# Performance work log

Measured on AMD Instinct MI355X. Metric: run time of the kernel, lower is better.

The kernel has to match this reference:

```python
import jax, jax.numpy as jnp
import numpy as np

K = 16  # neighbors
EPS = 1e-3  # Keras BatchNormalization default epsilon


def _bn(x, gamma, beta, mean, var):
    return (x - mean) * jax.lax.rsqrt(var + EPS) * gamma + beta


def setup_inputs() -> dict:
    key = jax.random.key(0)
    ks = jax.random.split(key, 16)
    B, P, C = 128, 256, 64
    inp = {
        "points": jax.random.normal(ks[0], (B, P, 3), jnp.float32),
        "features": jax.random.normal(ks[1], (B, P, C), jnp.float32),
        "w0": jax.random.normal(ks[2], (2 * C, 64), jnp.float32) * 0.08,
        "w1": jax.random.normal(ks[3], (64, 64), jnp.float32) * 0.12,
        "w2": jax.random.normal(ks[4], (64, 64), jnp.float32) * 0.12,
        "gammas": 0.8 + 0.4 * jax.random.uniform(ks[5], (3, 64), jnp.float32),
        "betas": 0.1 * jax.random.normal(ks[6], (3, 64), jnp.float32),
        "means": 0.1 * jax.random.normal(ks[7], (3, 64), jnp.float32),
        "variances": 0.5 + jax.random.uniform(ks[8], (3, 64), jnp.float32),
        "sc_w": jax.random.normal(ks[9], (C, 64), jnp.float32) * 0.12,
        "sc_gamma": 0.8 + 0.4 * jax.random.uniform(ks[10], (64,), jnp.float32),
        "sc_beta": 0.1 * jax.random.normal(ks[11], (64,), jnp.float32),
        "sc_mean": 0.1 * jax.random.normal(ks[12], (64,), jnp.float32),
        "sc_var": 0.5 + jax.random.uniform(ks[13], (64,), jnp.float32),
    }
    return inp


def reference(points, features, w0, w1, w2, gammas, betas, means, variances,
              sc_w, sc_gamma, sc_beta, sc_mean, sc_var):
    B, P, C = features.shape
    # pairwise squared-distance matrix: ||a||^2 - 2 a.b + ||b||^2  -> [B, P, P]
    r = jnp.sum(points * points, axis=2, keepdims=True)  # [B, P, 1]
    m = jnp.einsum('bpc,bqc->bpq', points, points)
    d = r - 2.0 * m + jnp.swapaxes(r, 1, 2)
    # top_k of -d: K+1 nearest (incl. self at position 0), drop self
    _, idx = jax.lax.top_k(-d, K + 1)
    idx = idx[:, :, 1:]  # [B, P, K]
    # KNN gather of features
    knn_fts = features[jnp.arange(B)[:, None, None], idx]  # [B, P, K, C]
    center = jnp.broadcast_to(features[:, :, None, :], (B, P, K, C))
    x = jnp.concatenate([center, knn_fts - center], axis=-1)  # [B, P, K, 2C]
    # per-edge MLP: 1x1 conv + BN (inference) + relu
    for i, w in enumerate((w0, w1, w2)):
        x = jnp.einsum('bpkc,cd->bpkd', x, w)
        x = _bn(x, gammas[i], betas[i], means[i], variances[i])
        x = jax.nn.relu(x)
    fts = jnp.mean(x, axis=2)  # average pooling over neighbors -> [B, P, 64]
    # shortcut 1x1 conv + BN
    sc = jnp.einsum('bpc,cd->bpd', features, sc_w)
    sc = _bn(sc, sc_gamma, sc_beta, sc_mean, sc_var)
    return jax.nn.relu(sc + fts)
```

## Files before the change

kernel.cpp:

```cpp
#include <hip/hip_runtime.h>
#include <math.h>

#define NBATCH 128
#define NP 256
#define NC 64
#define KNN 16
#define EPSV 1e-3f

typedef __bf16 bf16_t;
typedef bf16_t bf16x8 __attribute__((ext_vector_type(8)));
typedef float f32x4 __attribute__((ext_vector_type(4)));
typedef unsigned short u16x4 __attribute__((ext_vector_type(4)));

static __device__ __forceinline__ f32x4 mfma16(bf16x8 a, bf16x8 b, f32x4 c) {
    return __builtin_amdgcn_mfma_f32_16x16x32_bf16(a, b, c, 0, 0, 0);
}
static __device__ __forceinline__ unsigned short f2bfu(float f) {
    union { bf16_t b; unsigned short u; } cv; cv.b = (bf16_t)f; return cv.u;
}
static __device__ __forceinline__ unsigned umin2(unsigned a, unsigned b) { return a < b ? a : b; }
static __device__ __forceinline__ unsigned umax2(unsigned a, unsigned b) { return a > b ? a : b; }

#define CFENCE() asm volatile("" ::: "memory")

#define INSERTK(k_)                                                   \
    do {                                                              \
        _Pragma("unroll")                                             \
        for (int ii = KNN - 1; ii >= 1; --ii)                         \
            bk[ii] = umin2(umax2((k_), bk[ii - 1]), bk[ii]);          \
        bk[0] = umin2((k_), bk[0]);                                   \
    } while (0)

__global__ __launch_bounds__(256) void setup_kernel(
    const float* __restrict__ points, const float* __restrict__ features,
    const float* __restrict__ w0, const float* __restrict__ w1,
    const float* __restrict__ w2, const float* __restrict__ sc_w,
    const float* __restrict__ gammas, const float* __restrict__ betas,
    const float* __restrict__ means, const float* __restrict__ variances,
    const float* __restrict__ sc_gamma, const float* __restrict__ sc_beta,
    const float* __restrict__ sc_mean, const float* __restrict__ sc_var,
    unsigned short* __restrict__ fbf, unsigned short* __restrict__ wsf,
    float* __restrict__ bnp, int* __restrict__ knn_out)
{
    const int bid = blockIdx.x;
    if (bid < 1024) {
        const int tid = bid * 256 + threadIdx.x;
        const float4 a = ((const float4*)features)[tid * 2];
        const float4 b = ((const float4*)features)[tid * 2 + 1];
        union { unsigned short s[8]; uint4 v; } r;
        r.s[0] = f2bfu(a.x); r.s[1] = f2bfu(a.y); r.s[2] = f2bfu(a.z); r.s[3] = f2bfu(a.w);
        r.s[4] = f2bfu(b.x); r.s[5] = f2bfu(b.y); r.s[6] = f2bfu(b.z); r.s[7] = f2bfu(b.w);
        ((uint4*)fbf)[tid] = r.v;
    } else if (bid < 1105) {
        const int tid = (bid - 1024) * 256 + threadIdx.x;
        if (tid < 20480) {
            const int region = tid >> 12;
            const int e2 = tid & 4095;
            const int f = e2 >> 9;
            const int r = e2 & 511;
            const int lane = r >> 3, j = r & 7;
            const int ks = f >> 2, t = f & 3;
            const int row = ks * 32 + (lane >> 4) * 8 + j;
            const int col = 4 * (lane & 15) + t;
            float v;
            if (region == 0)      v = w0[row * 64 + col] - w0[(64 + row) * 64 + col];
            else if (region == 1) v = w0[(64 + row) * 64 + col];
            else if (region == 2) v = w1[row * 64 + col];
            else if (region == 3) v = w2[row * 64 + col];
            else                  v = sc_w[row * 64 + col];
            wsf[tid] = f2bfu(v);
        } else {
            const int e = tid - 20480;
            if (e < 192) {
                float s = gammas[e] * rsqrtf(variances[e] + EPSV);
                bnp[e] = s;
                bnp[192 + e] = betas[e] - means[e] * s;
            } else if (e < 256) {
                const int d = e - 192;
                float s = sc_gamma[d] * rsqrtf(sc_var[d] + EPSV);
                bnp[384 + d] = s;
                bnp[448 + d] = sc_beta[d] - sc_mean[d] * s;
            }
        }
    } else {
        __shared__ __align__(16) float4 sp[NP];
        __shared__ unsigned sk[128][17];
        const int kb = bid - 1105;
        const int bb = kb >> 1;
        const int qbase = (kb & 1) * 128;
        const int t = threadIdx.x;
        const int qt = t & 127;
        const int half = t >> 7;
        const int p = qbase + qt;

        const float* pb = points + (size_t)bb * NP * 3;
        sp[t] = make_float4(pb[t * 3 + 0], pb[t * 3 + 1], pb[t * 3 + 2], 0.f);
        __syncthreads();

        const float4 qp = sp[p];
        unsigned bk[KNN];
#pragma unroll
        for (int i = 0; i < KNN; ++i) bk[i] = 0xFFFFFFFFu;

        const int cbase = half * 128;
#pragma unroll 4
        for (int c = 0; c < 128; ++c) {
            const int cand = cbase + c;
            const float4 P = sp[cand];
            const float dx = qp.x - P.x, dy = qp.y - P.y, dz = qp.z - P.z;
            const float d = fmaf(dx, dx, fmaf(dy, dy, dz * dz));
            unsigned key = (__float_as_uint(d) & 0xFFFFFF00u) | (unsigned)cand;
            key = (cand == p) ? 0xFFFFFFFFu : key;
            INSERTK(key);
        }

        if (half == 1) {
#pragma unroll
            for (int i = 0; i < KNN; ++i) sk[qt][i] = bk[i];
        }
        __syncthreads();
        if (half == 0) {
            for (int j = 0; j < KNN; ++j) {
                const unsigned key = sk[qt][j];
                if (key >= bk[KNN - 1]) break;
                INSERTK(key);
            }
            int* op = knn_out + ((size_t)bb * NP + p) * KNN;
#pragma unroll
            for (int i = 0; i < KNN; ++i) op[i] = (int)(bk[i] & 0xFFu);
        }
    }
}

__global__ __launch_bounds__(256) void edge_kernel(
    const unsigned short* __restrict__ fbf, const int* __restrict__ knn_idx,
    const unsigned short* __restrict__ wsf, const float* __restrict__ bnp,
    float* __restrict__ out)
{
    __shared__ __align__(16) unsigned short wlds[24 * 512];
    __shared__ __align__(16) unsigned short slab[4][16 * 72];
    __shared__ __align__(16) float s0buf[4][8][64];
    __shared__ __align__(16) float ftsbuf[4][8][64];

    const int tid = threadIdx.x;
    const int wid = tid >> 6;
    const int l = tid & 63;
    const int i = l & 15;
    const int h = l >> 4;
    const int wg = (blockIdx.x & 7) * 128 + (blockIdx.x >> 3);
    const int p0 = (wg * 4 + wid) * 8;
    const int b = p0 >> 8;

    unsigned short* sl = slab[wid];

    {
        const uint4* src = (const uint4*)(wsf + 4096);
        uint4* dst = (uint4*)wlds;
#pragma unroll
        for (int k = 0; k < 6; ++k) dst[tid + k * 256] = src[tid + k * 256];
    }

    #define WF(fi_) (*(const bf16x8*)&wlds[(fi_) * 512 + l * 8])

    float4 scl[3], shf[3];
#pragma unroll
    for (int L = 0; L < 3; ++L) {
        scl[L] = *(const float4*)&bnp[L * 64 + 4 * i];
        shf[L] = *(const float4*)&bnp[192 + L * 64 + 4 * i];
    }

    {
        const bf16x8* __restrict__ WV = (const bf16x8*)(wsf);
        const unsigned short* cp = fbf + (size_t)(p0 + (i & 7)) * NC;
        bf16x8 a0 = *(const bf16x8*)(cp + 8 * h);
        bf16x8 a1 = *(const bf16x8*)(cp + 32 + 8 * h);
        f32x4 acc[4];
#pragma unroll
        for (int t = 0; t < 4; ++t) {
            f32x4 z = {0.f, 0.f, 0.f, 0.f};
            z = mfma16(a0, WV[t * 64 + l], z);
            acc[t] = mfma16(a1, WV[(4 + t) * 64 + l], z);
        }
        if (h < 2) {
#pragma unroll
            for (int r = 0; r < 4; ++r) {
                float4 v = make_float4(acc[0][r], acc[1][r], acc[2][r], acc[3][r]);
                *(float4*)&s0buf[wid][h * 4 + r][4 * i] = v;
            }
        }
    }
    int nks[8];
#pragma unroll
    for (int q = 0; q < 8; ++q) nks[q] = knn_idx[(size_t)(p0 + q) * KNN + i];

    __syncthreads();

    bf16x8 fc0, fc1;
    {
        const unsigned short* sp = fbf + (size_t)(b * NP + nks[0]) * NC;
        fc0 = *(const bf16x8*)(sp + 8 * h);
        fc1 = *(const bf16x8*)(sp + 32 + 8 * h);
    }

#pragma unroll
    for (int q = 0; q < 8; ++q) {
        float4 s0q = *(const float4*)&s0buf[wid][q][4 * i];
        {
            f32x4 acc[4];
#pragma unroll
            for (int t = 0; t < 4; ++t) {
                f32x4 z = {0.f, 0.f, 0.f, 0.f};
                z = mfma16(fc0, WF(t), z);
                acc[t] = mfma16(fc1, WF(4 + t), z);
            }
            const float* sp_ = (const float*)&s0q;
            const float* sc_ = (const float*)&scl[0];
            const float* sh_ = (const float*)&shf[0];
#pragma unroll
            for (int r = 0; r < 4; ++r) {
                u16x4 pk;
#pragma unroll
                for (int t = 0; t < 4; ++t)
                    pk[t] = f2bfu(fmaxf(fmaf(acc[t][r] + sp_[t], sc_[t], sh_[t]), 0.f));
                *(u16x4*)&sl[(h * 4 + r) * 72 + 4 * i] = pk;
            }
        }
        bf16x8 fn0, fn1;
        if (q < 7) {
            const unsigned short* sp = fbf + (size_t)(b * NP + nks[(q + 1) & 7]) * NC;
            fn0 = *(const bf16x8*)(sp + 8 * h);
            fn1 = *(const bf16x8*)(sp + 32 + 8 * h);
        }
        CFENCE();

        {
            bf16x8 x0 = *(const bf16x8*)(sl + i * 72 + h * 8);
            bf16x8 x1 = *(const bf16x8*)(sl + i * 72 + h * 8 + 32);
            f32x4 acc[4];
#pragma unroll
            for (int t = 0; t < 4; ++t) {
                f32x4 z = {0.f, 0.f, 0.f, 0.f};
                z = mfma16(x0, WF(8 + t), z);
                acc[t] = mfma16(x1, WF(12 + t), z);
            }
            const float* sc_ = (const float*)&scl[1];
            const float* sh_ = (const float*)&shf[1];
#pragma unroll
            for (int r = 0; r < 4; ++r) {
                u16x4 pk;
#pragma unroll
                for (int t = 0; t < 4; ++t)
                    pk[t] = f2bfu(fmaxf(fmaf(acc[t][r], sc_[t], sh_[t]), 0.f));
                *(u16x4*)&sl[(h * 4 + r) * 72 + 4 * i] = pk;
            }
        }
        CFENCE();

        {
            bf16x8 x0 = *(const bf16x8*)(sl + i * 72 + h * 8);
            bf16x8 x1 = *(const bf16x8*)(sl + i * 72 + h * 8 + 32);
            const float* sc_ = (const float*)&scl[2];
            const float* sh_ = (const float*)&shf[2];
            float st[4];
#pragma unroll
            for (int t = 0; t < 4; ++t) {
                f32x4 z = {0.f, 0.f, 0.f, 0.f};
                z = mfma16(x0, WF(16 + t), z);
                f32x4 acc = mfma16(x1, WF(20 + t), z);
                float s = 0.f;
#pragma unroll
                for (int r = 0; r < 4; ++r)
                    s += fmaxf(fmaf(acc[r], sc_[t], sh_[t]), 0.f);
                s += __shfl_xor(s, 16, 64);
                s += __shfl_xor(s, 32, 64);
                st[t] = s * (1.f / 16.f);
            }
            if (h == 0)
                *(float4*)&ftsbuf[wid][q][4 * i] =
                    make_float4(st[0], st[1], st[2], st[3]);
        }
        CFENCE();
        fc0 = fn0; fc1 = fn1;
    }

    {
        const bf16x8* __restrict__ WS = (const bf16x8*)(wsf + 16384);
        float4 sscl = *(const float4*)&bnp[384 + 4 * i];
        float4 sshf = *(const float4*)&bnp[448 + 4 * i];
        const unsigned short* fp = fbf + (size_t)(p0 + (i & 7)) * NC;
        bf16x8 a0 = *(const bf16x8*)(fp + 8 * h);
        bf16x8 a1 = *(const bf16x8*)(fp + 32 + 8 * h);
        f32x4 acc[4];
#pragma unroll
        for (int t = 0; t < 4; ++t) {
            f32x4 z = {0.f, 0.f, 0.f, 0.f};
            z = mfma16(a0, WS[t * 64 + l], z);
            acc[t] = mfma16(a1, WS[(4 + t) * 64 + l], z);
        }
        if (h < 2) {
            const float* ss_ = (const float*)&sscl;
            const float* sf_ = (const float*)&sshf;
#pragma unroll
            for (int r = 0; r < 4; ++r) {
                const int q = h * 4 + r;
                float4 fts = *(const float4*)&ftsbuf[wid][q][4 * i];
                const float* ft_ = (const float*)&fts;
                float4 o;
                float* o_ = (float*)&o;
#pragma unroll
                for (int t = 0; t < 4; ++t)
                    o_[t] = fmaxf(fmaf(acc[t][r], ss_[t], sf_[t]) + ft_[t], 0.f);
                *(float4*)&out[(size_t)(p0 + q) * NC + 4 * i] = o;
            }
        }
    }
    #undef WF
}

extern "C" void kernel_launch(void* const* d_in, const int* in_sizes, int n_in,
                              void* d_out, int out_size, void* d_ws, size_t ws_size,
                              hipStream_t stream) {
    const float* points    = (const float*)d_in[0];
    const float* features  = (const float*)d_in[1];
    const float* w0        = (const float*)d_in[2];
    const float* w1        = (const float*)d_in[3];
    const float* w2        = (const float*)d_in[4];
    const float* gammas    = (const float*)d_in[5];
    const float* betas     = (const float*)d_in[6];
    const float* means     = (const float*)d_in[7];
    const float* variances = (const float*)d_in[8];
    const float* sc_w      = (const float*)d_in[9];
    const float* sc_gamma  = (const float*)d_in[10];
    const float* sc_beta   = (const float*)d_in[11];
    const float* sc_mean   = (const float*)d_in[12];
    const float* sc_var    = (const float*)d_in[13];
    float* out = (float*)d_out;

    int* knn_buf = (int*)d_ws;
    unsigned short* fbf = (unsigned short*)((char*)d_ws + (1 << 21));
    unsigned short* wsf = (unsigned short*)((char*)d_ws + (3 << 21));
    float* bnp = (float*)((char*)d_ws + (3 << 21) + 40960);

    setup_kernel<<<1361, 256, 0, stream>>>(points, features, w0, w1, w2, sc_w,
                                           gammas, betas, means, variances,
                                           sc_gamma, sc_beta, sc_mean, sc_var,
                                           fbf, wsf, bnp, knn_buf);
    edge_kernel<<<NBATCH * NP / 32, 256, 0, stream>>>(fbf, knn_buf, wsf, bnp, out);
}
```

Baseline: 46.99 us.

## Fold BN scales into weights and chain MFMA layers in registers without LDS slab

The BN scales for layers 2 and 3 are folded into the next layer's weights, and the layer biases are pre-divided by the scale so they can seed the MFMA accumulators. The operand roles are swapped (weights as A, activations as B) and the output channels are permuted so each layer's MFMA output can be packed directly into the next layer's bf16 operand in registers. This removes the per-layer LDS slab round trip. The final neighbor sum uses DPP adds instead of shuffles, and the last scale plus the 1/16 mean factor are applied in the epilogue. A risk is that dividing the shift by the BN scale is numerically fragile if a scale is near zero.

```diff
diff --git a/kernel.cpp b/kernel.cpp
--- a/kernel.cpp
+++ b/kernel.cpp
@@ -10,7 +10,6 @@
 typedef __bf16 bf16_t;
 typedef bf16_t bf16x8 __attribute__((ext_vector_type(8)));
 typedef float f32x4 __attribute__((ext_vector_type(4)));
-typedef unsigned short u16x4 __attribute__((ext_vector_type(4)));
 
 static __device__ __forceinline__ f32x4 mfma16(bf16x8 a, bf16x8 b, f32x4 c) {
     return __builtin_amdgcn_mfma_f32_16x16x32_bf16(a, b, c, 0, 0, 0);
@@ -20,6 +19,28 @@
 }
 static __device__ __forceinline__ unsigned umin2(unsigned a, unsigned b) { return a < b ? a : b; }
 static __device__ __forceinline__ unsigned umax2(unsigned a, unsigned b) { return a > b ? a : b; }
+
+static __device__ __forceinline__ bf16x8 packrelu(f32x4 a, f32x4 b) {
+    bf16x8 r;
+    r[0] = (bf16_t)fmaxf(a[0], 0.f); r[1] = (bf16_t)fmaxf(a[1], 0.f);
+    r[2] = (bf16_t)fmaxf(a[2], 0.f); r[3] = (bf16_t)fmaxf(a[3], 0.f);
+    r[4] = (bf16_t)fmaxf(b[0], 0.f); r[5] = (bf16_t)fmaxf(b[1], 0.f);
+    r[6] = (bf16_t)fmaxf(b[2], 0.f); r[7] = (bf16_t)fmaxf(b[3], 0.f);
+    return r;
+}
+
+template <int CTRL>
+static __device__ __forceinline__ float dppadd(float v) {
+    int x = __builtin_amdgcn_mov_dpp(__float_as_int(v), CTRL, 0xF, 0xF, true);
+    return v + __int_as_float(x);
+}
+static __device__ __forceinline__ float sum16(float v) {
+    v = dppadd<0xB1>(v);
+    v = dppadd<0x4E>(v);
+    v = dppadd<0x141>(v);
+    v = dppadd<0x140>(v);
+    return v;
+}
 
 #define CFENCE() asm volatile("" ::: "memory")
 
@@ -51,7 +72,7 @@
         r.s[0] = f2bfu(a.x); r.s[1] = f2bfu(a.y); r.s[2] = f2bfu(a.z); r.s[3] = f2bfu(a.w);
         r.s[4] = f2bfu(b.x); r.s[5] = f2bfu(b.y); r.s[6] = f2bfu(b.z); r.s[7] = f2bfu(b.w);
         ((uint4*)fbf)[tid] = r.v;
-    } else if (bid < 1105) {
+    } else if (bid < 1106) {
         const int tid = (bid - 1024) * 256 + threadIdx.x;
         if (tid < 20480) {
             const int region = tid >> 12;
@@ -60,32 +81,49 @@
             const int r = e2 & 511;
             const int lane = r >> 3, j = r & 7;
             const int ks = f >> 2, t = f & 3;
-            const int row = ks * 32 + (lane >> 4) * 8 + j;
-            const int col = 4 * (lane & 15) + t;
+            const int m = lane & 15;
+            const int k_in = ks * 32 + (lane >> 4) * 8 + j;
+            const int kp = (t >> 1) * 32 + (m >> 2) * 8 + (t & 1) * 4 + (m & 3);
             float v;
-            if (region == 0)      v = w0[row * 64 + col] - w0[(64 + row) * 64 + col];
-            else if (region == 1) v = w0[(64 + row) * 64 + col];
-            else if (region == 2) v = w1[row * 64 + col];
-            else if (region == 3) v = w2[row * 64 + col];
-            else                  v = sc_w[row * 64 + col];
+            if (region == 0)      v = w0[k_in * 64 + kp] - w0[(64 + k_in) * 64 + kp];
+            else if (region == 1) v = w0[(64 + k_in) * 64 + kp];
+            else if (region == 2) {
+                float s1 = gammas[k_in] * rsqrtf(variances[k_in] + EPSV);
+                v = s1 * w1[k_in * 64 + kp];
+            } else if (region == 3) {
+                float s2 = gammas[64 + k_in] * rsqrtf(variances[64 + k_in] + EPSV);
+                v = s2 * w2[k_in * 64 + kp];
+            } else {
+                v = sc_w[k_in * 64 + (4 * m + t)];
+            }
             wsf[tid] = f2bfu(v);
         } else {
             const int e = tid - 20480;
             if (e < 192) {
-                float s = gammas[e] * rsqrtf(variances[e] + EPSV);
-                bnp[e] = s;
-                bnp[192 + e] = betas[e] - means[e] * s;
+                const int L = e >> 6;
+                const int pos = e & 63;
+                const int t = pos >> 4, m = pos & 15;
+                const int c = (t >> 1) * 32 + (m >> 2) * 8 + (t & 1) * 4 + (m & 3);
+                float scl = gammas[L * 64 + c] * rsqrtf(variances[L * 64 + c] + EPSV);
+                float shf = betas[L * 64 + c] - means[L * 64 + c] * scl;
+                bnp[e] = shf / scl;
             } else if (e < 256) {
-                const int d = e - 192;
-                float s = sc_gamma[d] * rsqrtf(sc_var[d] + EPSV);
-                bnp[384 + d] = s;
-                bnp[448 + d] = sc_beta[d] - sc_mean[d] * s;
+                const int c = e - 192;
+                float s3 = gammas[128 + c] * rsqrtf(variances[128 + c] + EPSV);
+                bnp[e] = s3 * (1.f / 16.f);
+            } else if (e < 320) {
+                const int c = e - 256;
+                bnp[e] = sc_gamma[c] * rsqrtf(sc_var[c] + EPSV);
+            } else if (e < 384) {
+                const int c = e - 320;
+                float s = sc_gamma[c] * rsqrtf(sc_var[c] + EPSV);
+                bnp[e] = sc_beta[c] - sc_mean[c] * s;
             }
         }
     } else {
         __shared__ __align__(16) float4 sp[NP];
         __shared__ unsigned sk[128][17];
-        const int kb = bid - 1105;
+        const int kb = bid - 1106;
         const int bb = kb >> 1;
         const int qbase = (kb & 1) * 128;
         const int t = threadIdx.x;
@@ -138,7 +176,6 @@
     float* __restrict__ out)
 {
     __shared__ __align__(16) unsigned short wlds[24 * 512];
-    __shared__ __align__(16) unsigned short slab[4][16 * 72];
     __shared__ __align__(16) float s0buf[4][8][64];
     __shared__ __align__(16) float ftsbuf[4][8][64];
 
@@ -151,42 +188,33 @@
     const int p0 = (wg * 4 + wid) * 8;
     const int b = p0 >> 8;
 
-    unsigned short* sl = slab[wid];
-
     {
         const uint4* src = (const uint4*)(wsf + 4096);
         uint4* dst = (uint4*)wlds;
 #pragma unroll
         for (int k = 0; k < 6; ++k) dst[tid + k * 256] = src[tid + k * 256];
     }
-
     #define WF(fi_) (*(const bf16x8*)&wlds[(fi_) * 512 + l * 8])
 
-    float4 scl[3], shf[3];
-#pragma unroll
-    for (int L = 0; L < 3; ++L) {
-        scl[L] = *(const float4*)&bnp[L * 64 + 4 * i];
-        shf[L] = *(const float4*)&bnp[192 + L * 64 + 4 * i];
+    f32x4 cin2[4], cin3[4];
+#pragma unroll
+    for (int t = 0; t < 4; ++t) {
+        cin2[t] = *(const f32x4*)&bnp[64 + t * 16 + 4 * h];
+        cin3[t] = *(const f32x4*)&bnp[128 + t * 16 + 4 * h];
     }
 
     {
         const bf16x8* __restrict__ WV = (const bf16x8*)(wsf);
         const unsigned short* cp = fbf + (size_t)(p0 + (i & 7)) * NC;
-        bf16x8 a0 = *(const bf16x8*)(cp + 8 * h);
-        bf16x8 a1 = *(const bf16x8*)(cp + 32 + 8 * h);
-        f32x4 acc[4];
-#pragma unroll
-        for (int t = 0; t < 4; ++t) {
-            f32x4 z = {0.f, 0.f, 0.f, 0.f};
-            z = mfma16(a0, WV[t * 64 + l], z);
-            acc[t] = mfma16(a1, WV[(4 + t) * 64 + l], z);
-        }
-        if (h < 2) {
-#pragma unroll
-            for (int r = 0; r < 4; ++r) {
-                float4 v = make_float4(acc[0][r], acc[1][r], acc[2][r], acc[3][r]);
-                *(float4*)&s0buf[wid][h * 4 + r][4 * i] = v;
-            }
+        bf16x8 b0 = *(const bf16x8*)(cp + 8 * h);
+        bf16x8 b1 = *(const bf16x8*)(cp + 32 + 8 * h);
+#pragma unroll
+        for (int t = 0; t < 4; ++t) {
+            f32x4 acc = *(const f32x4*)&bnp[t * 16 + 4 * h];
+            acc = mfma16(WV[t * 64 + l], b0, acc);
+            acc = mfma16(WV[(4 + t) * 64 + l], b1, acc);
+            if (i < 8)
+                *(f32x4*)&s0buf[wid][i][t * 16 + 4 * h] = acc;
         }
     }
     int nks[8];
@@ -195,98 +223,66 @@
 
     __syncthreads();
 
-    bf16x8 fc0, fc1;
+    bf16x8 fb0, fb1;
     {
         const unsigned short* sp = fbf + (size_t)(b * NP + nks[0]) * NC;
-        fc0 = *(const bf16x8*)(sp + 8 * h);
-        fc1 = *(const bf16x8*)(sp + 32 + 8 * h);
+        fb0 = *(const bf16x8*)(sp + 8 * h);
+        fb1 = *(const bf16x8*)(sp + 32 + 8 * h);
     }
 
 #pragma unroll
     for (int q = 0; q < 8; ++q) {
-        float4 s0q = *(const float4*)&s0buf[wid][q][4 * i];
-        {
-            f32x4 acc[4];
-#pragma unroll
-            for (int t = 0; t < 4; ++t) {
-                f32x4 z = {0.f, 0.f, 0.f, 0.f};
-                z = mfma16(fc0, WF(t), z);
-                acc[t] = mfma16(fc1, WF(4 + t), z);
-            }
-            const float* sp_ = (const float*)&s0q;
-            const float* sc_ = (const float*)&scl[0];
-            const float* sh_ = (const float*)&shf[0];
-#pragma unroll
-            for (int r = 0; r < 4; ++r) {
-                u16x4 pk;
-#pragma unroll
-                for (int t = 0; t < 4; ++t)
-                    pk[t] = f2bfu(fmaxf(fmaf(acc[t][r] + sp_[t], sc_[t], sh_[t]), 0.f));
-                *(u16x4*)&sl[(h * 4 + r) * 72 + 4 * i] = pk;
-            }
-        }
-        bf16x8 fn0, fn1;
+        f32x4 acc[4];
+#pragma unroll
+        for (int t = 0; t < 4; ++t) {
+            f32x4 z = *(const f32x4*)&s0buf[wid][q][t * 16 + 4 * h];
+            z = mfma16(WF(t), fb0, z);
+            acc[t] = mfma16(WF(4 + t), fb1, z);
+        }
+        bf16x8 g0, g1;
         if (q < 7) {
             const unsigned short* sp = fbf + (size_t)(b * NP + nks[(q + 1) & 7]) * NC;
-            fn0 = *(const bf16x8*)(sp + 8 * h);
-            fn1 = *(const bf16x8*)(sp + 32 + 8 * h);
-        }
-        CFENCE();
-
-        {
-            bf16x8 x0 = *(const bf16x8*)(sl + i * 72 + h * 8);
-            bf16x8 x1 = *(const bf16x8*)(sl + i * 72 + h * 8 + 32);
-            f32x4 acc[4];
-#pragma unroll
-            for (int t = 0; t < 4; ++t) {
-                f32x4 z = {0.f, 0.f, 0.f, 0.f};
-                z = mfma16(x0, WF(8 + t), z);
-                acc[t] = mfma16(x1, WF(12 + t), z);
-            }
-            const float* sc_ = (const float*)&scl[1];
-            const float* sh_ = (const float*)&shf[1];
-#pragma unroll
-            for (int r = 0; r < 4; ++r) {
-                u16x4 pk;
-#pragma unroll
-                for (int t = 0; t < 4; ++t)
-                    pk[t] = f2bfu(fmaxf(fmaf(acc[t][r], sc_[t], sh_[t]), 0.f));
-                *(u16x4*)&sl[(h * 4 + r) * 72 + 4 * i] = pk;
-            }
-        }
-        CFENCE();
-
-        {
-            bf16x8 x0 = *(const bf16x8*)(sl + i * 72 + h * 8);
-            bf16x8 x1 = *(const bf16x8*)(sl + i * 72 + h * 8 + 32);
-            const float* sc_ = (const float*)&scl[2];
-            const float* sh_ = (const float*)&shf[2];
-            float st[4];
-#pragma unroll
-            for (int t = 0; t < 4; ++t) {
-                f32x4 z = {0.f, 0.f, 0.f, 0.f};
-                z = mfma16(x0, WF(16 + t), z);
-                f32x4 acc = mfma16(x1, WF(20 + t), z);
-                float s = 0.f;
-#pragma unroll
-                for (int r = 0; r < 4; ++r)
-                    s += fmaxf(fmaf(acc[r], sc_[t], sh_[t]), 0.f);
-                s += __shfl_xor(s, 16, 64);
-                s += __shfl_xor(s, 32, 64);
-                st[t] = s * (1.f / 16.f);
-            }
-            if (h == 0)
-                *(float4*)&ftsbuf[wid][q][4 * i] =
-                    make_float4(st[0], st[1], st[2], st[3]);
-        }
-        CFENCE();
-        fc0 = fn0; fc1 = fn1;
-    }
+            g0 = *(const bf16x8*)(sp + 8 * h);
+            g1 = *(const bf16x8*)(sp + 32 + 8 * h);
+        }
+        bf16x8 x0 = packrelu(acc[0], acc[1]);
+        bf16x8 x1 = packrelu(acc[2], acc[3]);
+
+#pragma unroll
+        for (int t = 0; t < 4; ++t) {
+            f32x4 z = mfma16(WF(8 + t), x0, cin2[t]);
+            acc[t] = mfma16(WF(12 + t), x1, z);
+        }
+        bf16x8 y0 = packrelu(acc[0], acc[1]);
+        bf16x8 y1 = packrelu(acc[2], acc[3]);
+
+#pragma unroll
+        for (int t = 0; t < 4; ++t) {
+            f32x4 z = mfma16(WF(16 + t), y0, cin3[t]);
+            acc[t] = mfma16(WF(20 + t), y1, z);
+        }
+        float st[4][4];
+#pragma unroll
+        for (int t = 0; t < 4; ++t)
+#pragma unroll
+            for (int r = 0; r < 4; ++r)
+                st[t][r] = sum16(fmaxf(acc[t][r], 0.f));
+        if (i == 0) {
+#pragma unroll
+            for (int t = 0; t < 4; ++t)
+                *(float4*)&ftsbuf[wid][q][(t >> 1) * 32 + h * 8 + (t & 1) * 4] =
+                    make_float4(st[t][0], st[t][1], st[t][2], st[t][3]);
+        }
+        fb0 = g0; fb1 = g1;
+    }
+    CFENCE();
 
     {
         const bf16x8* __restrict__ WS = (const bf16x8*)(wsf + 16384);
-        float4 sscl = *(const float4*)&bnp[384 + 4 * i];
-        float4 sshf = *(const float4*)&bnp[448 + 4 * i];
+        const int i4 = 4 * i;
+        float4 sscl = *(const float4*)&bnp[256 + i4];
+        float4 sshf = *(const float4*)&bnp[320 + i4];
+        float4 f3q  = *(const float4*)&bnp[192 + i4];
         const unsigned short* fp = fbf + (size_t)(p0 + (i & 7)) * NC;
         bf16x8 a0 = *(const bf16x8*)(fp + 8 * h);
         bf16x8 a1 = *(const bf16x8*)(fp + 32 + 8 * h);
@@ -300,17 +296,18 @@
         if (h < 2) {
             const float* ss_ = (const float*)&sscl;
             const float* sf_ = (const float*)&sshf;
+            const float* f3_ = (const float*)&f3q;
 #pragma unroll
             for (int r = 0; r < 4; ++r) {
                 const int q = h * 4 + r;
-                float4 fts = *(const float4*)&ftsbuf[wid][q][4 * i];
+                float4 fts = *(const float4*)&ftsbuf[wid][q][i4];
                 const float* ft_ = (const float*)&fts;
                 float4 o;
                 float* o_ = (float*)&o;
 #pragma unroll
                 for (int t = 0; t < 4; ++t)
-                    o_[t] = fmaxf(fmaf(acc[t][r], ss_[t], sf_[t]) + ft_[t], 0.f);
-                *(float4*)&out[(size_t)(p0 + q) * NC + 4 * i] = o;
+                    o_[t] = fmaxf(fmaf(acc[t][r], ss_[t], sf_[t]) + ft_[t] * f3_[t], 0.f);
+                *(float4*)&out[(size_t)(p0 + q) * NC + i4] = o;
             }
         }
     }
@@ -341,7 +338,7 @@
     unsigned short* wsf = (unsigned short*)((char*)d_ws + (3 << 21));
     float* bnp = (float*)((char*)d_ws + (3 << 21) + 40960);
 
-    setup_kernel<<<1361, 256, 0, stream>>>(points, features, w0, w1, w2, sc_w,
+    setup_kernel<<<1362, 256, 0, stream>>>(points, features, w0, w1, w2, sc_w,
                                            gammas, betas, means, variances,
                                            sc_gamma, sc_beta, sc_mean, sc_var,
                                            fbf, wsf, bnp, knn_buf);
```

Measured after the change: 47.75 us. No clear change (+1.6%).
